# Kernel optimization log

Measured on AMD Instinct MI355X. Metric: run time of the kernel, lower is better.

The kernel has to match this reference:

```python
import jax, jax.numpy as jnp
import numpy as np

EMBED_DIM = 1024
NUM_HEADS = 16
HEAD_DIM = EMBED_DIM // NUM_HEADS


def setup_inputs() -> dict:
    key = jax.random.key(0)
    ks = jax.random.split(key, 12)
    B, S, D = 4, 2048, EMBED_DIM
    scale = 1.0 / np.sqrt(D)
    inp = {
        "query": jax.random.normal(ks[0], (B, S, D), jnp.float32),
        "key": jax.random.normal(ks[1], (B, S, D), jnp.float32),
        "value": jax.random.normal(ks[2], (B, S, D), jnp.float32),
        # nn.Linear weights: [out_features, in_features], y = x @ W.T + b
        "Wq": jax.random.normal(ks[3], (D, D), jnp.float32) * scale,
        "bq": jnp.zeros((D,), jnp.float32),
        "Wk": jax.random.normal(ks[4], (D, D), jnp.float32) * scale,
        "bk": jnp.zeros((D,), jnp.float32),
        "Wv": jax.random.normal(ks[5], (D, D), jnp.float32) * scale,
        "bv": jnp.zeros((D,), jnp.float32),
        "Wo": jax.random.normal(ks[6], (D, D), jnp.float32) * scale,
        "bo": jnp.zeros((D,), jnp.float32),
    }
    return inp


def reference(query, key, value, Wq, bq, Wk, bk, Wv, bv, Wo, bo):
    B, Sq, D = query.shape
    Sk = key.shape[1]
    H, Dh = NUM_HEADS, HEAD_DIM

    def proj(x, W, b):
        # [B,S,D] -> [B,H,S,Dh]
        y = jnp.einsum('bsd,ed->bse', x, W) + b
        return y.reshape(x.shape[0], x.shape[1], H, Dh).transpose(0, 2, 1, 3)

    q = proj(query, Wq, bq)
    k = proj(key, Wk, bk)
    v = proj(value, Wv, bv)

    # sigmoid attention (no softmax); dropout is identity in eval mode
    scores = jnp.einsum('bhqd,bhkd->bhqk', q, k) / jnp.sqrt(jnp.float32(Dh)).astype(q.dtype)
    attn = jax.nn.sigmoid(scores)
    out = jnp.einsum('bhqk,bhkd->bhqd', attn, v)

    out = out.transpose(0, 2, 1, 3).reshape(B, Sq, D)
    return jnp.einsum('bsd,ed->bse', out, Wo) + bo
```

## Files before the change

kernel.cpp:

```cpp
#include <hip/hip_runtime.h>


typedef _Float16 f16x4 __attribute__((ext_vector_type(4)));
typedef _Float16 f16x8 __attribute__((ext_vector_type(8)));
typedef float    f32x4 __attribute__((ext_vector_type(4)));

typedef __attribute__((address_space(3))) void* lds_vp;
typedef const __attribute__((address_space(1))) void* gbl_vp;

__device__ __forceinline__ void gld_lds16(const void* g, void* l) {
  __builtin_amdgcn_global_load_lds((gbl_vp)g, (lds_vp)l, 16, 0, 0);
}

__device__ __forceinline__ f16x8 cvt8(float4 a, float4 b) {
  return (f16x8){(_Float16)a.x, (_Float16)a.y, (_Float16)a.z, (_Float16)a.w,
                 (_Float16)b.x, (_Float16)b.y, (_Float16)b.z, (_Float16)b.w};
}

#define BM 128
#define BN 128
#define BK 32


template <bool AF16, bool BF16, bool TRANSV, bool OUTF32>
__global__ __launch_bounds__(256) void gemm_bt(const void* __restrict__ Av,
                                               const void* __restrict__ Bv,
                                               const float* __restrict__ bias,
                                               void* __restrict__ Yv,
                                               int M, int N, int K) {
  __shared__ __align__(16) _Float16 sA[BM * BK];
  __shared__ __align__(16) _Float16 sB[BN * BK];

  const int t = threadIdx.x, lane = t & 63, wid = t >> 6;
  const int m0 = blockIdx.x * BM, n0 = blockIdx.y * BN;
  const int wm = (wid >> 1) * 64, wn = (wid & 1) * 64;
  const int lrow = lane & 15, g = lane >> 4;

  f32x4 acc[4][4] = {};

  const int arow = 16 * wid + (lane >> 2);
  const int gq = (lane & 3) ^ ((lane >> 3) & 3);
  _Float16* lA1 = sA + wid * 512;
  _Float16* lA2 = sA + 2048 + wid * 512;
  _Float16* lB1 = sB + wid * 512;
  _Float16* lB2 = sB + 2048 + wid * 512;

  const int mrow = t >> 1, mhalf = t & 1;
  const int mm = (mrow >> 1) & 3;
  const int ch_lo = mrow * 4 + ((2 * mhalf) ^ mm);
  const int ch_hi = ch_lo ^ 1;

  const _Float16* pA16a = nullptr; const _Float16* pA16b = nullptr;
  const float* pA32 = nullptr;
  if constexpr (AF16) {
    const _Float16* A = (const _Float16*)Av;
    pA16a = A + (size_t)(m0 + arow) * K + gq * 8;
    pA16b = A + (size_t)(m0 + 64 + arow) * K + gq * 8;
  } else {
    pA32 = (const float*)Av + (size_t)(m0 + mrow) * K + mhalf * 16;
  }
  const _Float16* pB16a = nullptr; const _Float16* pB16b = nullptr;
  const float* pB32 = nullptr;
  if constexpr (BF16) {
    const _Float16* B = (const _Float16*)Bv;
    pB16a = B + (size_t)(n0 + arow) * K + gq * 8;
    pB16b = B + (size_t)(n0 + 64 + arow) * K + gq * 8;
  } else {
    pB32 = (const float*)Bv + (size_t)(n0 + mrow) * K + mhalf * 16;
  }

  const int xr = g ^ ((lrow >> 1) & 3);

  for (int k0 = 0; k0 < K; k0 += BK) {
    float4 av[4], bv4[4];
    if constexpr (!AF16) {
      const float4* p = (const float4*)(pA32 + k0);
      av[0] = p[0]; av[1] = p[1]; av[2] = p[2]; av[3] = p[3];
    }
    if constexpr (!BF16) {
      const float4* p = (const float4*)(pB32 + k0);
      bv4[0] = p[0]; bv4[1] = p[1]; bv4[2] = p[2]; bv4[3] = p[3];
    }
    __syncthreads();
    if constexpr (AF16) {
      gld_lds16(pA16a + k0, lA1);
      gld_lds16(pA16b + k0, lA2);
    } else {
      *(f16x8*)(sA + ch_lo * 8) = cvt8(av[0], av[1]);
      *(f16x8*)(sA + ch_hi * 8) = cvt8(av[2], av[3]);
    }
    if constexpr (BF16) {
      gld_lds16(pB16a + k0, lB1);
      gld_lds16(pB16b + k0, lB2);
    } else {
      *(f16x8*)(sB + ch_lo * 8) = cvt8(bv4[0], bv4[1]);
      *(f16x8*)(sB + ch_hi * 8) = cvt8(bv4[2], bv4[3]);
    }
    __syncthreads();

    f16x8 af[4], bf[4];
#pragma unroll
    for (int i = 0; i < 4; i++)
      af[i] = *(const f16x8*)(sA + (wm + i * 16 + lrow) * 32 + xr * 8);
#pragma unroll
    for (int j = 0; j < 4; j++)
      bf[j] = *(const f16x8*)(sB + (wn + j * 16 + lrow) * 32 + xr * 8);
#pragma unroll
    for (int i = 0; i < 4; i++)
#pragma unroll
      for (int j = 0; j < 4; j++)
        acc[i][j] = __builtin_amdgcn_mfma_f32_16x16x32_f16(af[i], bf[j], acc[i][j], 0, 0, 0);
  }

  const int orow = g * 4, ocol = lrow;
#pragma unroll
  for (int j = 0; j < 4; j++) {
    const int col = n0 + wn + j * 16 + ocol;
    const float bv = bias[col];
#pragma unroll
    for (int i = 0; i < 4; i++) {
      const int row = m0 + wm + i * 16 + orow;
      if constexpr (TRANSV) {
        _Float16* VT = (_Float16*)Yv;
        _Float16* dst = VT + (((size_t)(row >> 11) * 16 + (col >> 6)) * 64 + (col & 63)) * 2048 +
                        (row & 2047);
        f16x4 v = {(_Float16)(acc[i][j][0] + bv), (_Float16)(acc[i][j][1] + bv),
                   (_Float16)(acc[i][j][2] + bv), (_Float16)(acc[i][j][3] + bv)};
        *(f16x4*)dst = v;
      } else if constexpr (OUTF32) {
        float* Y = (float*)Yv;
#pragma unroll
        for (int r = 0; r < 4; r++) Y[(size_t)(row + r) * N + col] = acc[i][j][r] + bv;
      } else {
        _Float16* Y = (_Float16*)Yv;
#pragma unroll
        for (int r = 0; r < 4; r++) Y[(size_t)(row + r) * N + col] = (_Float16)(acc[i][j][r] + bv);
      }
    }
  }
}

#define LDA 72

__global__ __launch_bounds__(256, 4) void attn_sig(const _Float16* __restrict__ Q,
                                                   const _Float16* __restrict__ K,
                                                   const _Float16* __restrict__ VT,
                                                   _Float16* __restrict__ O) {
  __shared__ __align__(16) _Float16 sK[64 * LDA];
  __shared__ __align__(16) _Float16 sVT[64 * LDA];
  __shared__ __align__(16) _Float16 sP[4][32 * LDA];

  const int t = threadIdx.x, lane = t & 63, wid = t >> 6;
  const int b = blockIdx.z, h = blockIdx.y, q0 = blockIdx.x * 128;
  const int lrow = lane & 15, g = lane >> 4;
  const int qw = q0 + wid * 32;

  f16x8 qf[2][2];
#pragma unroll
  for (int gr = 0; gr < 2; gr++) {
    const _Float16* qp = Q + (size_t)(b * 2048 + qw + gr * 16 + lrow) * 1024 + h * 64;
    qf[gr][0] = *(const f16x8*)(qp + g * 8);
    qf[gr][1] = *(const f16x8*)(qp + 32 + g * 8);
  }

  f32x4 oacc[2][4] = {};
  const int srow = t >> 2, scol = (t & 3) * 16;
  const _Float16* vtb = VT + ((size_t)(b * 16 + h) * 64 + srow) * 2048;

  for (int kt = 0; kt < 2048; kt += 64) {
    const _Float16* kp = K + (size_t)(b * 2048 + kt + srow) * 1024 + h * 64 + scol;
    uint4 ka = *(const uint4*)kp, kb = *(const uint4*)(kp + 8);
    const _Float16* vp = vtb + kt + scol;
    uint4 va = *(const uint4*)vp, vb = *(const uint4*)(vp + 8);
    __syncthreads();
    *(uint4*)&sK[srow * LDA + scol] = ka;
    *(uint4*)&sK[srow * LDA + scol + 8] = kb;
    *(uint4*)&sVT[srow * LDA + scol] = va;
    *(uint4*)&sVT[srow * LDA + scol + 8] = vb;
    __syncthreads();

#pragma unroll
    for (int gr = 0; gr < 2; gr++) {
      f32x4 sacc[4] = {};
#pragma unroll
      for (int j = 0; j < 4; j++) {
        f16x8 kf0 = *(const f16x8*)&sK[(j * 16 + lrow) * LDA + g * 8];
        f16x8 kf1 = *(const f16x8*)&sK[(j * 16 + lrow) * LDA + 32 + g * 8];
        sacc[j] = __builtin_amdgcn_mfma_f32_16x16x32_f16(kf0, qf[gr][0], sacc[j], 0, 0, 0);
        sacc[j] = __builtin_amdgcn_mfma_f32_16x16x32_f16(kf1, qf[gr][1], sacc[j], 0, 0, 0);
      }
#pragma unroll
      for (int j = 0; j < 4; j++) {
        f16x4 p4;
#pragma unroll
        for (int r = 0; r < 4; r++) {
          float e = __expf(sacc[j][r] * -0.125f);
          p4[r] = (_Float16)__builtin_amdgcn_rcpf(1.0f + e);
        }
        *(f16x4*)&sP[wid][(gr * 16 + lrow) * LDA + j * 16 + g * 4] = p4;
      }
    }
#pragma unroll
    for (int kk = 0; kk < 2; kk++) {
      f16x8 pf0 = *(const f16x8*)&sP[wid][(lrow) * LDA + kk * 32 + g * 8];
      f16x8 pf1 = *(const f16x8*)&sP[wid][(16 + lrow) * LDA + kk * 32 + g * 8];
#pragma unroll
      for (int j = 0; j < 4; j++) {
        f16x8 vf = *(const f16x8*)&sVT[(j * 16 + lrow) * LDA + kk * 32 + g * 8];
        oacc[0][j] = __builtin_amdgcn_mfma_f32_16x16x32_f16(pf0, vf, oacc[0][j], 0, 0, 0);
        oacc[1][j] = __builtin_amdgcn_mfma_f32_16x16x32_f16(pf1, vf, oacc[1][j], 0, 0, 0);
      }
    }
  }

#pragma unroll
  for (int gr = 0; gr < 2; gr++)
#pragma unroll
    for (int j = 0; j < 4; j++)
#pragma unroll
      for (int r = 0; r < 4; r++)
        O[(size_t)(b * 2048 + qw + gr * 16 + g * 4 + r) * 1024 + h * 64 + j * 16 + lrow] =
            (_Float16)oacc[gr][j][r];
}

struct CvtArgs {
  const float* src[7];
  _Float16* dst[7];
  int n[7];
  int cnt;
};

__global__ __launch_bounds__(256) void cvt_f32_f16(CvtArgs a) {
  const int ti = blockIdx.y;
  if (ti >= a.cnt) return;
  const int i = (blockIdx.x * 256 + threadIdx.x) * 8;
  if (i >= a.n[ti]) return;
  const float4* s = (const float4*)(a.src[ti] + i);
  float4 x = s[0], y = s[1];
  *(f16x8*)(a.dst[ti] + i) = cvt8(x, y);
}

extern "C" void kernel_launch(void* const* d_in, const int* in_sizes, int n_in,
                              void* d_out, int out_size, void* d_ws, size_t ws_size,
                              hipStream_t stream) {
  const float* query = (const float*)d_in[0];
  const float* key   = (const float*)d_in[1];
  const float* value = (const float*)d_in[2];
  const float* Wq = (const float*)d_in[3];
  const float* bq = (const float*)d_in[4];
  const float* Wk = (const float*)d_in[5];
  const float* bk = (const float*)d_in[6];
  const float* Wv = (const float*)d_in[7];
  const float* bv = (const float*)d_in[8];
  const float* Wo = (const float*)d_in[9];
  const float* bo = (const float*)d_in[10];
  float* out = (float*)d_out;

  const int D = 1024, M = 8192;
  const size_t MB = 1024 * 1024;
  char* ws = (char*)d_ws;
  dim3 bb(256), gg(M / BM, D / BN), ga(16, 16, 4);

  if (ws_size >= 104 * MB) {
    _Float16* Xq = (_Float16*)(ws + 0 * MB);
    _Float16* Xk = (_Float16*)(ws + 16 * MB);
    _Float16* Xv = (_Float16*)(ws + 32 * MB);
    _Float16* Qp = (_Float16*)(ws + 48 * MB);
    _Float16* Kp = (_Float16*)(ws + 64 * MB);
    _Float16* VT = (_Float16*)(ws + 80 * MB);
    _Float16* Wf = (_Float16*)(ws + 96 * MB);
    _Float16* AO = Xq;
    CvtArgs ca{};
    ca.src[0] = query; ca.dst[0] = Xq; ca.n[0] = M * D;
    ca.src[1] = key;   ca.dst[1] = Xk; ca.n[1] = M * D;
    ca.src[2] = value; ca.dst[2] = Xv; ca.n[2] = M * D;
    ca.src[3] = Wq; ca.dst[3] = Wf + 0 * 1048576; ca.n[3] = D * D;
    ca.src[4] = Wk; ca.dst[4] = Wf + 1 * 1048576; ca.n[4] = D * D;
    ca.src[5] = Wv; ca.dst[5] = Wf + 2 * 1048576; ca.n[5] = D * D;
    ca.src[6] = Wo; ca.dst[6] = Wf + 3 * 1048576; ca.n[6] = D * D;
    ca.cnt = 7;
    cvt_f32_f16<<<dim3(4096, 7), bb, 0, stream>>>(ca);
    gemm_bt<true, true, false, false><<<gg, bb, 0, stream>>>(Xq, Wf + 0 * 1048576, bq, Qp, M, D, D);
    gemm_bt<true, true, false, false><<<gg, bb, 0, stream>>>(Xk, Wf + 1 * 1048576, bk, Kp, M, D, D);
    gemm_bt<true, true, true,  false><<<gg, bb, 0, stream>>>(Xv, Wf + 2 * 1048576, bv, VT, M, D, D);
    attn_sig<<<ga, bb, 0, stream>>>(Qp, Kp, VT, AO);
    gemm_bt<true, true, false, true><<<gg, bb, 0, stream>>>(AO, Wf + 3 * 1048576, bo, out, M, D, D);
  } else if (ws_size >= 72 * MB) {
    _Float16* Wf = (_Float16*)(ws + 0 * MB);
    _Float16* Qp = (_Float16*)(ws + 8 * MB);
    _Float16* Kp = (_Float16*)(ws + 24 * MB);
    _Float16* VT = (_Float16*)(ws + 40 * MB);
    _Float16* AO = (_Float16*)(ws + 56 * MB);
    CvtArgs ca{};
    ca.src[0] = Wq; ca.dst[0] = Wf + 0 * 1048576; ca.n[0] = D * D;
    ca.src[1] = Wk; ca.dst[1] = Wf + 1 * 1048576; ca.n[1] = D * D;
    ca.src[2] = Wv; ca.dst[2] = Wf + 2 * 1048576; ca.n[2] = D * D;
    ca.src[3] = Wo; ca.dst[3] = Wf + 3 * 1048576; ca.n[3] = D * D;
    ca.cnt = 4;
    cvt_f32_f16<<<dim3(512, 4), bb, 0, stream>>>(ca);
    gemm_bt<false, true, false, false><<<gg, bb, 0, stream>>>(query, Wf + 0 * 1048576, bq, Qp, M, D, D);
    gemm_bt<false, true, false, false><<<gg, bb, 0, stream>>>(key,   Wf + 1 * 1048576, bk, Kp, M, D, D);
    gemm_bt<false, true, true,  false><<<gg, bb, 0, stream>>>(value, Wf + 2 * 1048576, bv, VT, M, D, D);
    attn_sig<<<ga, bb, 0, stream>>>(Qp, Kp, VT, AO);
    gemm_bt<true, true, false, true><<<gg, bb, 0, stream>>>(AO, Wf + 3 * 1048576, bo, out, M, D, D);
  } else {
    _Float16* Qp = (_Float16*)(ws + 0 * MB);
    _Float16* Kp = (_Float16*)(ws + 16 * MB);
    _Float16* VT = (_Float16*)(ws + 32 * MB);
    _Float16* AO = (_Float16*)(ws + 48 * MB);
    gemm_bt<false, false, false, false><<<gg, bb, 0, stream>>>(query, Wq, bq, Qp, M, D, D);
    gemm_bt<false, false, false, false><<<gg, bb, 0, stream>>>(key,   Wk, bk, Kp, M, D, D);
    gemm_bt<false, false, true,  false><<<gg, bb, 0, stream>>>(value, Wv, bv, VT, M, D, D);
    attn_sig<<<ga, bb, 0, stream>>>(Qp, Kp, VT, AO);
    gemm_bt<true, false, false, true><<<gg, bb, 0, stream>>>(AO, Wo, bo, out, M, D, D);
  }
}
```

Measured before the change: 388.5 us.

## Use 32x32 MFMA attention with register P, fuse QKV GEMMs, permute VT

Rewrites the attention kernel to use 32x32 MFMA tiles with 64 queries per wave. The sigmoid probabilities stay in registers and feed a 32x32x8 MFMA directly, which removes the LDS round-trip for P. To make that register layout match, the V projection writes VT with a permuted sequence index. The three Q/K/V projection GEMMs are merged into one launch, output is staged through LDS for coalesced stores, and the mid-size workspace path is removed. Occupancy drops to 2 blocks per CU and register pressure rises.

```diff
diff --git a/kernel.cpp b/kernel.cpp
--- a/kernel.cpp
+++ b/kernel.cpp
@@ -4,6 +4,7 @@
 typedef _Float16 f16x4 __attribute__((ext_vector_type(4)));
 typedef _Float16 f16x8 __attribute__((ext_vector_type(8)));
 typedef float    f32x4 __attribute__((ext_vector_type(4)));
+typedef float    f32x16 __attribute__((ext_vector_type(16)));
 
 typedef __attribute__((address_space(3))) void* lds_vp;
 typedef const __attribute__((address_space(1))) void* gbl_vp;
@@ -122,8 +123,9 @@
       const int row = m0 + wm + i * 16 + orow;
       if constexpr (TRANSV) {
         _Float16* VT = (_Float16*)Yv;
-        _Float16* dst = VT + (((size_t)(row >> 11) * 16 + (col >> 6)) * 64 + (col & 63)) * 2048 +
-                        (row & 2047);
+        int s = row & 2047;
+        int sp = (s & ~12) | ((s & 4) << 1) | ((s & 8) >> 1);
+        _Float16* dst = VT + (((size_t)(row >> 11) * 16 + (col >> 6)) * 64 + (col & 63)) * 2048 + sp;
         f16x4 v = {(_Float16)(acc[i][j][0] + bv), (_Float16)(acc[i][j][1] + bv),
                    (_Float16)(acc[i][j][2] + bv), (_Float16)(acc[i][j][3] + bv)};
         *(f16x4*)dst = v;
@@ -140,87 +142,195 @@
   }
 }
 
-#define LDA 72
-
-__global__ __launch_bounds__(256, 4) void attn_sig(const _Float16* __restrict__ Q,
+__global__ __launch_bounds__(256) void qkv_gemm(const _Float16* __restrict__ Xq,
+                                                const _Float16* __restrict__ Xk,
+                                                const _Float16* __restrict__ Xv,
+                                                const _Float16* __restrict__ W,
+                                                const float* __restrict__ bq,
+                                                const float* __restrict__ bk,
+                                                const float* __restrict__ bv,
+                                                _Float16* __restrict__ Qo,
+                                                _Float16* __restrict__ Ko,
+                                                _Float16* __restrict__ VT) {
+  __shared__ __align__(16) _Float16 sA[BM * BK];
+  __shared__ __align__(16) _Float16 sB[BN * BK];
+
+  const int t = threadIdx.x, lane = t & 63, wid = t >> 6;
+  const int n0g = blockIdx.x * BN, m0 = blockIdx.y * BM;
+  const int seg = blockIdx.x >> 3, n0 = n0g & 1023;
+  const _Float16* A = (seg == 0) ? Xq : (seg == 1) ? Xk : Xv;
+  const float* bias = (seg == 0) ? bq : (seg == 1) ? bk : bv;
+  const int K = 1024;
+
+  const int wm = (wid >> 1) * 64, wn = (wid & 1) * 64;
+  const int lrow = lane & 15, g = lane >> 4;
+
+  f32x4 acc[4][4] = {};
+
+  const int arow = 16 * wid + (lane >> 2);
+  const int gq = (lane & 3) ^ ((lane >> 3) & 3);
+  _Float16* lA1 = sA + wid * 512;
+  _Float16* lA2 = sA + 2048 + wid * 512;
+  _Float16* lB1 = sB + wid * 512;
+  _Float16* lB2 = sB + 2048 + wid * 512;
+
+  const _Float16* pA16a = A + (size_t)(m0 + arow) * K + gq * 8;
+  const _Float16* pA16b = A + (size_t)(m0 + 64 + arow) * K + gq * 8;
+  const _Float16* pB16a = W + (size_t)(n0g + arow) * K + gq * 8;
+  const _Float16* pB16b = W + (size_t)(n0g + 64 + arow) * K + gq * 8;
+
+  const int xr = g ^ ((lrow >> 1) & 3);
+
+  for (int k0 = 0; k0 < K; k0 += BK) {
+    __syncthreads();
+    gld_lds16(pA16a + k0, lA1);
+    gld_lds16(pA16b + k0, lA2);
+    gld_lds16(pB16a + k0, lB1);
+    gld_lds16(pB16b + k0, lB2);
+    __syncthreads();
+
+    f16x8 af[4], bf[4];
+#pragma unroll
+    for (int i = 0; i < 4; i++)
+      af[i] = *(const f16x8*)(sA + (wm + i * 16 + lrow) * 32 + xr * 8);
+#pragma unroll
+    for (int j = 0; j < 4; j++)
+      bf[j] = *(const f16x8*)(sB + (wn + j * 16 + lrow) * 32 + xr * 8);
+#pragma unroll
+    for (int i = 0; i < 4; i++)
+#pragma unroll
+      for (int j = 0; j < 4; j++)
+        acc[i][j] = __builtin_amdgcn_mfma_f32_16x16x32_f16(af[i], bf[j], acc[i][j], 0, 0, 0);
+  }
+
+  const int orow = g * 4, ocol = lrow;
+#pragma unroll
+  for (int j = 0; j < 4; j++) {
+    const int col = n0 + wn + j * 16 + ocol;
+    const float bvv = bias[col];
+#pragma unroll
+    for (int i = 0; i < 4; i++) {
+      const int row = m0 + wm + i * 16 + orow;
+      if (seg == 2) {
+        int s = row & 2047;
+        int sp = (s & ~12) | ((s & 4) << 1) | ((s & 8) >> 1);
+        _Float16* dst = VT + (((size_t)(row >> 11) * 16 + (col >> 6)) * 64 + (col & 63)) * 2048 + sp;
+        f16x4 v = {(_Float16)(acc[i][j][0] + bvv), (_Float16)(acc[i][j][1] + bvv),
+                   (_Float16)(acc[i][j][2] + bvv), (_Float16)(acc[i][j][3] + bvv)};
+        *(f16x4*)dst = v;
+      } else {
+        _Float16* Y = (seg == 0) ? Qo : Ko;
+#pragma unroll
+        for (int r = 0; r < 4; r++) Y[(size_t)(row + r) * 1024 + col] = (_Float16)(acc[i][j][r] + bvv);
+      }
+    }
+  }
+}
+
+#define LDS_ROW 72
+
+__global__ __launch_bounds__(256, 2) void attn_sig(const _Float16* __restrict__ Q,
                                                    const _Float16* __restrict__ K,
                                                    const _Float16* __restrict__ VT,
                                                    _Float16* __restrict__ O) {
-  __shared__ __align__(16) _Float16 sK[64 * LDA];
-  __shared__ __align__(16) _Float16 sVT[64 * LDA];
-  __shared__ __align__(16) _Float16 sP[4][32 * LDA];
+  __shared__ __align__(16) _Float16 smem[256 * LDS_ROW];
+  _Float16* sK = smem;
+  _Float16* sVT = smem + 64 * LDS_ROW;
 
   const int t = threadIdx.x, lane = t & 63, wid = t >> 6;
-  const int b = blockIdx.z, h = blockIdx.y, q0 = blockIdx.x * 128;
-  const int lrow = lane & 15, g = lane >> 4;
-  const int qw = q0 + wid * 32;
-
-  f16x8 qf[2][2];
-#pragma unroll
-  for (int gr = 0; gr < 2; gr++) {
-    const _Float16* qp = Q + (size_t)(b * 2048 + qw + gr * 16 + lrow) * 1024 + h * 64;
-    qf[gr][0] = *(const f16x8*)(qp + g * 8);
-    qf[gr][1] = *(const f16x8*)(qp + 32 + g * 8);
-  }
-
-  f32x4 oacc[2][4] = {};
+  const int l31 = lane & 31, g5 = lane >> 5;
+  const int b = blockIdx.z, h = blockIdx.y, q0 = blockIdx.x * 256;
+  const int qw = q0 + wid * 64;
+
+  f16x8 qf[2][4];
+#pragma unroll
+  for (int qt = 0; qt < 2; qt++) {
+    const _Float16* qp = Q + (size_t)(b * 2048 + qw + qt * 32 + l31) * 1024 + h * 64;
+#pragma unroll
+    for (int dhc = 0; dhc < 4; dhc++) qf[qt][dhc] = *(const f16x8*)(qp + dhc * 16 + g5 * 8);
+  }
+
+  f32x16 oacc[2][2] = {};
+
   const int srow = t >> 2, scol = (t & 3) * 16;
-  const _Float16* vtb = VT + ((size_t)(b * 16 + h) * 64 + srow) * 2048;
+  const _Float16* kbase = K + ((size_t)(b * 2048) + srow) * 1024 + h * 64 + scol;
+  const _Float16* vbase = VT + ((size_t)((b * 16 + h) * 64 + srow)) * 2048 + scol;
 
   for (int kt = 0; kt < 2048; kt += 64) {
-    const _Float16* kp = K + (size_t)(b * 2048 + kt + srow) * 1024 + h * 64 + scol;
-    uint4 ka = *(const uint4*)kp, kb = *(const uint4*)(kp + 8);
-    const _Float16* vp = vtb + kt + scol;
-    uint4 va = *(const uint4*)vp, vb = *(const uint4*)(vp + 8);
-    __syncthreads();
-    *(uint4*)&sK[srow * LDA + scol] = ka;
-    *(uint4*)&sK[srow * LDA + scol + 8] = kb;
-    *(uint4*)&sVT[srow * LDA + scol] = va;
-    *(uint4*)&sVT[srow * LDA + scol + 8] = vb;
-    __syncthreads();
-
-#pragma unroll
-    for (int gr = 0; gr < 2; gr++) {
-      f32x4 sacc[4] = {};
-#pragma unroll
-      for (int j = 0; j < 4; j++) {
-        f16x8 kf0 = *(const f16x8*)&sK[(j * 16 + lrow) * LDA + g * 8];
-        f16x8 kf1 = *(const f16x8*)&sK[(j * 16 + lrow) * LDA + 32 + g * 8];
-        sacc[j] = __builtin_amdgcn_mfma_f32_16x16x32_f16(kf0, qf[gr][0], sacc[j], 0, 0, 0);
-        sacc[j] = __builtin_amdgcn_mfma_f32_16x16x32_f16(kf1, qf[gr][1], sacc[j], 0, 0, 0);
+    uint4 ka = *(const uint4*)(kbase + (size_t)kt * 1024);
+    uint4 kb = *(const uint4*)(kbase + (size_t)kt * 1024 + 8);
+    uint4 va = *(const uint4*)(vbase + kt);
+    uint4 vb = *(const uint4*)(vbase + kt + 8);
+    __syncthreads();
+    *(uint4*)&sK[srow * LDS_ROW + scol] = ka;
+    *(uint4*)&sK[srow * LDS_ROW + scol + 8] = kb;
+    *(uint4*)&sVT[srow * LDS_ROW + scol] = va;
+    *(uint4*)&sVT[srow * LDS_ROW + scol + 8] = vb;
+    __syncthreads();
+
+#pragma unroll
+    for (int kt32 = 0; kt32 < 2; kt32++) {
+      f16x8 kf[4];
+#pragma unroll
+      for (int dhc = 0; dhc < 4; dhc++)
+        kf[dhc] = *(const f16x8*)&sK[(kt32 * 32 + l31) * LDS_ROW + dhc * 16 + g5 * 8];
+
+      f16x4 p16[2][4];
+#pragma unroll
+      for (int qt = 0; qt < 2; qt++) {
+        f32x16 sacc = {};
+#pragma unroll
+        for (int dhc = 0; dhc < 4; dhc++)
+          sacc = __builtin_amdgcn_mfma_f32_32x32x16_f16(kf[dhc], qf[qt][dhc], sacc, 0, 0, 0);
+#pragma unroll
+        for (int c = 0; c < 4; c++) {
+          f16x4 p4;
+#pragma unroll
+          for (int r = 0; r < 4; r++) {
+            float e = __expf(sacc[4 * c + r] * -0.125f);
+            p4[r] = (_Float16)__builtin_amdgcn_rcpf(1.0f + e);
+          }
+          p16[qt][c] = p4;
+        }
       }
-#pragma unroll
-      for (int j = 0; j < 4; j++) {
-        f16x4 p4;
-#pragma unroll
-        for (int r = 0; r < 4; r++) {
-          float e = __expf(sacc[j][r] * -0.125f);
-          p4[r] = (_Float16)__builtin_amdgcn_rcpf(1.0f + e);
+
+#pragma unroll
+      for (int dht = 0; dht < 2; dht++)
+#pragma unroll
+        for (int tloc = 0; tloc < 2; tloc++) {
+          f16x8 vfr = *(const f16x8*)&sVT[(dht * 32 + l31) * LDS_ROW + kt32 * 32 + tloc * 16 + g5 * 8];
+          f16x4 vlo = __builtin_shufflevector(vfr, vfr, 0, 1, 2, 3);
+          f16x4 vhi = __builtin_shufflevector(vfr, vfr, 4, 5, 6, 7);
+#pragma unroll
+          for (int qt = 0; qt < 2; qt++) {
+            oacc[qt][dht] = __builtin_amdgcn_mfma_f32_32x32x8f16(vlo, p16[qt][tloc * 2 + 0],
+                                                                 oacc[qt][dht], 0, 0, 0);
+            oacc[qt][dht] = __builtin_amdgcn_mfma_f32_32x32x8f16(vhi, p16[qt][tloc * 2 + 1],
+                                                                 oacc[qt][dht], 0, 0, 0);
+          }
         }
-        *(f16x4*)&sP[wid][(gr * 16 + lrow) * LDA + j * 16 + g * 4] = p4;
+    }
+  }
+
+  __syncthreads();
+  _Float16* ep = smem;
+#pragma unroll
+  for (int qt = 0; qt < 2; qt++)
+#pragma unroll
+    for (int dht = 0; dht < 2; dht++)
+#pragma unroll
+      for (int c = 0; c < 4; c++) {
+        f16x4 o4 = {(_Float16)oacc[qt][dht][4 * c + 0], (_Float16)oacc[qt][dht][4 * c + 1],
+                    (_Float16)oacc[qt][dht][4 * c + 2], (_Float16)oacc[qt][dht][4 * c + 3]};
+        *(f16x4*)&ep[(wid * 64 + qt * 32 + l31) * LDS_ROW + dht * 32 + c * 8 + g5 * 4] = o4;
       }
-    }
-#pragma unroll
-    for (int kk = 0; kk < 2; kk++) {
-      f16x8 pf0 = *(const f16x8*)&sP[wid][(lrow) * LDA + kk * 32 + g * 8];
-      f16x8 pf1 = *(const f16x8*)&sP[wid][(16 + lrow) * LDA + kk * 32 + g * 8];
-#pragma unroll
-      for (int j = 0; j < 4; j++) {
-        f16x8 vf = *(const f16x8*)&sVT[(j * 16 + lrow) * LDA + kk * 32 + g * 8];
-        oacc[0][j] = __builtin_amdgcn_mfma_f32_16x16x32_f16(pf0, vf, oacc[0][j], 0, 0, 0);
-        oacc[1][j] = __builtin_amdgcn_mfma_f32_16x16x32_f16(pf1, vf, oacc[1][j], 0, 0, 0);
-      }
-    }
-  }
-
-#pragma unroll
-  for (int gr = 0; gr < 2; gr++)
-#pragma unroll
-    for (int j = 0; j < 4; j++)
-#pragma unroll
-      for (int r = 0; r < 4; r++)
-        O[(size_t)(b * 2048 + qw + gr * 16 + g * 4 + r) * 1024 + h * 64 + j * 16 + lrow] =
-            (_Float16)oacc[gr][j][r];
+  __syncthreads();
+#pragma unroll
+  for (int i = 0; i < 8; i++) {
+    const int q = i * 32 + (t >> 3), dhc = t & 7;
+    f16x8 row = *(const f16x8*)&ep[q * LDS_ROW + dhc * 8];
+    *(f16x8*)(O + (size_t)(b * 2048 + q0 + q) * 1024 + h * 64 + dhc * 8) = row;
+  }
 }
 
 struct CvtArgs {
@@ -259,7 +369,7 @@
   const int D = 1024, M = 8192;
   const size_t MB = 1024 * 1024;
   char* ws = (char*)d_ws;
-  dim3 bb(256), gg(M / BM, D / BN), ga(16, 16, 4);
+  dim3 bb(256), ga(8, 16, 4);
 
   if (ws_size >= 104 * MB) {
     _Float16* Xq = (_Float16*)(ws + 0 * MB);
@@ -280,38 +390,18 @@
     ca.src[6] = Wo; ca.dst[6] = Wf + 3 * 1048576; ca.n[6] = D * D;
     ca.cnt = 7;
     cvt_f32_f16<<<dim3(4096, 7), bb, 0, stream>>>(ca);
-    gemm_bt<true, true, false, false><<<gg, bb, 0, stream>>>(Xq, Wf + 0 * 1048576, bq, Qp, M, D, D);
-    gemm_bt<true, true, false, false><<<gg, bb, 0, stream>>>(Xk, Wf + 1 * 1048576, bk, Kp, M, D, D);
-    gemm_bt<true, true, true,  false><<<gg, bb, 0, stream>>>(Xv, Wf + 2 * 1048576, bv, VT, M, D, D);
+    qkv_gemm<<<dim3(24, 64), bb, 0, stream>>>(Xq, Xk, Xv, Wf, bq, bk, bv, Qp, Kp, VT);
     attn_sig<<<ga, bb, 0, stream>>>(Qp, Kp, VT, AO);
-    gemm_bt<true, true, false, true><<<gg, bb, 0, stream>>>(AO, Wf + 3 * 1048576, bo, out, M, D, D);
-  } else if (ws_size >= 72 * MB) {
-    _Float16* Wf = (_Float16*)(ws + 0 * MB);
-    _Float16* Qp = (_Float16*)(ws + 8 * MB);
-    _Float16* Kp = (_Float16*)(ws + 24 * MB);
-    _Float16* VT = (_Float16*)(ws + 40 * MB);
-    _Float16* AO = (_Float16*)(ws + 56 * MB);
-    CvtArgs ca{};
-    ca.src[0] = Wq; ca.dst[0] = Wf + 0 * 1048576; ca.n[0] = D * D;
-    ca.src[1] = Wk; ca.dst[1] = Wf + 1 * 1048576; ca.n[1] = D * D;
-    ca.src[2] = Wv; ca.dst[2] = Wf + 2 * 1048576; ca.n[2] = D * D;
-    ca.src[3] = Wo; ca.dst[3] = Wf + 3 * 1048576; ca.n[3] = D * D;
-    ca.cnt = 4;
-    cvt_f32_f16<<<dim3(512, 4), bb, 0, stream>>>(ca);
-    gemm_bt<false, true, false, false><<<gg, bb, 0, stream>>>(query, Wf + 0 * 1048576, bq, Qp, M, D, D);
-    gemm_bt<false, true, false, false><<<gg, bb, 0, stream>>>(key,   Wf + 1 * 1048576, bk, Kp, M, D, D);
-    gemm_bt<false, true, true,  false><<<gg, bb, 0, stream>>>(value, Wf + 2 * 1048576, bv, VT, M, D, D);
-    attn_sig<<<ga, bb, 0, stream>>>(Qp, Kp, VT, AO);
-    gemm_bt<true, true, false, true><<<gg, bb, 0, stream>>>(AO, Wf + 3 * 1048576, bo, out, M, D, D);
+    gemm_bt<true, true, false, true><<<dim3(64, 8), bb, 0, stream>>>(AO, Wf + 3 * 1048576, bo, out, M, D, D);
   } else {
     _Float16* Qp = (_Float16*)(ws + 0 * MB);
     _Float16* Kp = (_Float16*)(ws + 16 * MB);
     _Float16* VT = (_Float16*)(ws + 32 * MB);
     _Float16* AO = (_Float16*)(ws + 48 * MB);
-    gemm_bt<false, false, false, false><<<gg, bb, 0, stream>>>(query, Wq, bq, Qp, M, D, D);
-    gemm_bt<false, false, false, false><<<gg, bb, 0, stream>>>(key,   Wk, bk, Kp, M, D, D);
-    gemm_bt<false, false, true,  false><<<gg, bb, 0, stream>>>(value, Wv, bv, VT, M, D, D);
+    gemm_bt<false, false, false, false><<<dim3(64, 8), bb, 0, stream>>>(query, Wq, bq, Qp, M, D, D);
+    gemm_bt<false, false, false, false><<<dim3(64, 8), bb, 0, stream>>>(key,   Wk, bk, Kp, M, D, D);
+    gemm_bt<false, false, true,  false><<<dim3(64, 8), bb, 0, stream>>>(value, Wv, bv, VT, M, D, D);
     attn_sig<<<ga, bb, 0, stream>>>(Qp, Kp, VT, AO);
-    gemm_bt<true, false, false, true><<<gg, bb, 0, stream>>>(AO, Wo, bo, out, M, D, D);
-  }
-}
+    gemm_bt<true, false, false, true><<<dim3(64, 8), bb, 0, stream>>>(AO, Wo, bo, out, M, D, D);
+  }
+}
```

New measurement: 379.5 us. 2.3% less time.
